# Performance work log

Hardware: AMD Instinct MI355X
Metric: run time of the kernel (lower is better)

The kernel has to match this reference:

```python
import jax, jax.numpy as jnp
import numpy as np

H, HD, C = 16, 64, 64            # num_heads, head_dim, mini_batch_size
BASE_LR = 1.0
EPS = 1e-6                        # ttt LN eps (ln_fwd / ln_fused_l2_bwd)


def _l2norm(x):
    return x / jnp.maximum(jnp.linalg.norm(x, axis=-1, keepdims=True), 1e-12)


def _ln_fwd(x, g, b):
    mu = x.mean(-1, keepdims=True)
    var = x.var(-1, keepdims=True)
    return g * ((x - mu) * jax.lax.rsqrt(var + EPS)) + b


def _ln_l2_bwd(x, tgt, g, b):
    # gradient of ||LN(x)*g+b - tgt||^2 / 2 wrt x
    D = x.shape[-1]
    mu = x.mean(-1, keepdims=True)
    var = x.var(-1, keepdims=True)
    std = jnp.sqrt(var + EPS)
    xh = (x - mu) / std
    gout = (g * xh + b) - tgt
    gxh = gout * g
    return (D * gxh - gxh.sum(-1, keepdims=True) - xh * (gxh * xh).sum(-1, keepdims=True)) / (D * std)


def setup_inputs() -> dict:
    key = jax.random.key(0)
    ks = jax.random.split(key, 12)
    B, L, D = 4, 8192, 1024
    std = 0.02
    return {
        'hidden_states': jax.random.normal(ks[0], (B, L, D), jnp.float32),
        'wq_w': jax.random.normal(ks[1], (D, D), jnp.float32) * std,
        'wq_b': jnp.zeros((D,), jnp.float32),
        'wk_w': jax.random.normal(ks[2], (D, D), jnp.float32) * std,
        'wk_b': jnp.zeros((D,), jnp.float32),
        'wv_w': jax.random.normal(ks[3], (D, D), jnp.float32) * std,
        'wv_b': jnp.zeros((D,), jnp.float32),
        'wo_w': jax.random.normal(ks[4], (D, D), jnp.float32) * std,
        'wo_b': jnp.zeros((D,), jnp.float32),
        'ttt_norm_weight': jnp.ones((H, HD), jnp.float32),
        'ttt_norm_bias': jnp.zeros((H, HD), jnp.float32),
        'ttt_lr_weight': jax.random.normal(ks[5], (H, 1, D), jnp.float32) * std,
        'ttt_lr_bias': jnp.zeros((H, 1), jnp.float32),
        'W1': jax.random.normal(ks[6], (H, HD, HD), jnp.float32) * std,
        'b1': jnp.zeros((H, 1, HD), jnp.float32),
        'post_norm_w': jnp.ones((D,), jnp.float32),
        'post_norm_b': jnp.zeros((D,), jnp.float32),
    }


def _forward(hidden_states, wq_w, wq_b, wk_w, wk_b, wv_w, wv_b, wo_w, wo_b,
             ttt_norm_weight, ttt_norm_bias, ttt_lr_weight, ttt_lr_bias,
             W1, b1, post_norm_w, post_norm_b):
    B, L, D = hidden_states.shape
    NC = L // C
    XQ = (hidden_states @ wq_w.T + wq_b).reshape(B, L, H, HD)
    XK = (hidden_states @ wk_w.T + wk_b).reshape(B, L, H, HD)
    XV = (hidden_states @ wv_w.T + wv_b).reshape(B, L, H, HD)
    XQ = _l2norm(XQ)
    XK = _l2norm(XK)
    # ln_reconstruction_target (uses sample std, ddof=1, eps=1e-5 on std)
    d = XV - XK
    mu = d.mean(-1, keepdims=True)
    sd = d.std(-1, keepdims=True, ddof=1)
    XV = ttt_norm_weight[None, None] * ((d - mu) / (sd + 1e-5)) + ttt_norm_bias[None, None] + XK
    # reshape to mini-batches: [B,H,NC,C,HD]
    Xmb = hidden_states.reshape(B, NC, C, D)
    to_mb = lambda t: t.transpose(0, 2, 1, 3).reshape(B, H, NC, C, HD)
    XQ, XK, XV = to_mb(XQ), to_mb(XK), to_mb(XV)
    # eta: sigmoid lr gate per token, row-broadcast over mini-batch
    ttt_lr = jax.nn.sigmoid(jnp.einsum('bnkc,hdc->bhnkd', Xmb, ttt_lr_weight)
                            + ttt_lr_bias.reshape(1, H, 1, 1, 1))     # [B,H,NC,C,1]
    eta = jnp.swapaxes(ttt_lr, -1, -2) * (BASE_LR / HD / C)           # [B,H,NC,1,C]
    mask = jnp.tril(jnp.ones((C, C), hidden_states.dtype))
    g = ttt_norm_weight[None, :, None, :]
    bta = ttt_norm_bias[None, :, None, :]
    W0 = jnp.broadcast_to(W1[None], (B, H, HD, HD))
    b0 = jnp.broadcast_to(b1[None], (B, H, 1, HD))

    def step(carry, xs):
        W, bvec = carry
        xq, xk, xv, eta_row = xs                      # eta_row: [B,H,1,C]
        Z1 = xk @ W + bvec                            # [B,H,C,HD]
        grad = _ln_l2_bwd(Z1, xv - xk, g, bta)        # [B,H,C,HD]
        Attn = mask * jnp.einsum('bhid,bhjd->bhij', xq, xk)   # [B,H,C,C]
        eta_full = jnp.broadcast_to(eta_row, Attn.shape)      # [B,H,C,C]
        b1_bar = bvec - (mask * eta_full) @ grad              # [B,H,C,HD]
        Z1_bar = xq @ W - (eta_full * Attn) @ grad + b1_bar
        last_eta = eta_full[..., -1, :, None]                 # [B,H,C,1]
        W_new = W - jnp.einsum('bhcd,bhce->bhde', last_eta * xk, grad)
        b_new = bvec - (last_eta * grad).sum(-2, keepdims=True)
        out = xq + _ln_fwd(Z1_bar, g, bta)
        return (W_new, b_new), out

    xs = (jnp.moveaxis(XQ, 2, 0), jnp.moveaxis(XK, 2, 0),
          jnp.moveaxis(XV, 2, 0), jnp.moveaxis(eta, 2, 0))
    _, outs = jax.lax.scan(step, (W0, b0), xs)        # outs: [NC,B,H,C,HD]
    y = jnp.moveaxis(outs, 0, 2).reshape(B, H, L, HD).transpose(0, 2, 1, 3).reshape(B, L, D)
    # post LayerNorm (eps=1e-6) + output projection
    mu2 = y.mean(-1, keepdims=True)
    var2 = y.var(-1, keepdims=True)
    y = post_norm_w * ((y - mu2) * jax.lax.rsqrt(var2 + 1e-6)) + post_norm_b
    return y @ wo_w.T + wo_b


def reference(hidden_states, wq_w, wq_b, wk_w, wk_b, wv_w, wv_b, wo_w, wo_b,
              ttt_norm_weight, ttt_norm_bias, ttt_lr_weight, ttt_lr_bias,
              W1, b1, post_norm_w, post_norm_b):
    return _forward(hidden_states, wq_w, wq_b, wk_w, wk_b, wv_w, wv_b, wo_w, wo_b,
                    ttt_norm_weight, ttt_norm_bias, ttt_lr_weight, ttt_lr_bias,
                    W1, b1, post_norm_w, post_norm_b)
```

## Files before the change

### kernel.cpp

```cpp
#include <hip/hip_runtime.h>


typedef __attribute__((ext_vector_type(8))) short short8;
typedef __attribute__((ext_vector_type(4))) float f32x4;
typedef __attribute__((ext_vector_type(4))) unsigned short us4;

__device__ __forceinline__ float bf2f(unsigned short s) {
  union { unsigned int u; float f; } c;
  c.u = ((unsigned int)s) << 16;
  return c.f;
}
__device__ __forceinline__ unsigned short f2bf(float f) {
  union { float f; unsigned int u; } c;
  c.f = f;
  unsigned int u = c.u;
  return (unsigned short)((u + 0x7FFFu + ((u >> 16) & 1u)) >> 16);
}

__device__ __forceinline__ void gload_lds16(const void* g, void* l) {
  __builtin_amdgcn_global_load_lds(
      (const __attribute__((address_space(1))) unsigned int*)g,
      (__attribute__((address_space(3))) unsigned int*)l, 16, 0, 0);
}

__device__ __forceinline__ float dpp16_sum(float x) {
  int v = __float_as_int(x);
  x += __int_as_float(__builtin_amdgcn_update_dpp(v, v, 0xB1, 0xF, 0xF, true));
  v = __float_as_int(x);
  x += __int_as_float(__builtin_amdgcn_update_dpp(v, v, 0x4E, 0xF, 0xF, true));
  v = __float_as_int(x);
  x += __int_as_float(__builtin_amdgcn_update_dpp(v, v, 0x141, 0xF, 0xF, true));
  v = __float_as_int(x);
  x += __int_as_float(__builtin_amdgcn_update_dpp(v, v, 0x140, 0xF, 0xF, true));
  return x;
}

__device__ __forceinline__ void barrier_fast() {
  __builtin_amdgcn_sched_barrier(0);
  asm volatile("s_waitcnt lgkmcnt(0)" ::: "memory");
  __builtin_amdgcn_s_barrier();
  asm volatile("" ::: "memory");
  __builtin_amdgcn_sched_barrier(0);
}
__device__ __forceinline__ void bar_nowait() {
  __builtin_amdgcn_sched_barrier(0);
  asm volatile("" ::: "memory");
  __builtin_amdgcn_s_barrier();
  asm volatile("" ::: "memory");
  __builtin_amdgcn_sched_barrier(0);
}

__global__ __launch_bounds__(256) void cvt_f32_bf16(
    const float* __restrict__ in, unsigned short* __restrict__ out, long n) {
  long i = ((long)blockIdx.x * 256 + threadIdx.x) * 4;
  if (i + 3 < n) {
    float4 v = *(const float4*)&in[i];
    us4 o = { f2bf(v.x), f2bf(v.y), f2bf(v.z), f2bf(v.w) };
    *(us4*)&out[i] = o;
  }
}

__global__ __launch_bounds__(256) void build_wcat(
    const float* __restrict__ wq, const float* __restrict__ wk,
    const float* __restrict__ wv, const float* __restrict__ lrw,
    const float* __restrict__ wqb, const float* __restrict__ wkb,
    const float* __restrict__ wvb, const float* __restrict__ lrb,
    unsigned short* __restrict__ Wcat, float* __restrict__ biasc) {
  int i = blockIdx.x * 256 + threadIdx.x;
  int row = i >> 10, col = i & 1023;
  int h = row >> 8, o = row & 255;
  float v;
  if (o < 64)        v = wq[(h * 64 + o) * 1024 + col];
  else if (o < 128)  v = wk[(h * 64 + o - 64) * 1024 + col];
  else if (o < 192)  v = wv[(h * 64 + o - 128) * 1024 + col];
  else if (o == 192) v = lrw[h * 1024 + col];
  else               v = 0.f;
  Wcat[i] = f2bf(v);
  if (i < 4096) {
    int hh = i >> 8, oo = i & 255;
    float bv;
    if (oo < 64)        bv = wqb[hh * 64 + oo];
    else if (oo < 128)  bv = wkb[hh * 64 + oo - 64];
    else if (oo < 192)  bv = wvb[hh * 64 + oo - 128];
    else if (oo == 192) bv = lrb[hh];
    else                bv = 0.f;
    biasc[i] = bv;
  }
}


__global__ __launch_bounds__(512, 1) void gemm256_qkv(
    const unsigned short* __restrict__ A, const unsigned short* __restrict__ B,
    const float* __restrict__ bias, const float* __restrict__ tnw,
    const float* __restrict__ tnb, unsigned short* __restrict__ XQn,
    unsigned short* __restrict__ XKn, unsigned short* __restrict__ TGT,
    float* __restrict__ eta, long M, long K) {
  __shared__ __align__(16) unsigned short g_lds[49152];
  char* ldsc = (char*)g_lds;
  const int tid = threadIdx.x, lane = tid & 63, wid = tid >> 6;
  const int wm = wid >> 2, wn = wid & 3;
  const int l15 = lane & 15, lg = lane >> 4;
  const int NTILN = 16;

  unsigned nwg = gridDim.x, bid = blockIdx.x;
  unsigned cpx = nwg >> 3;
  unsigned swz = (bid & 7) * cpx + (bid >> 3);
  unsigned nidx = swz % (unsigned)NTILN, midx = swz / (unsigned)NTILN;
  const long m0 = (long)midx * 256, n0 = (long)nidx * 256;
  const long ldab = K * 2;

  const int srow = wid * 16 + (lane >> 2);
  const int scol = ((lane & 3) * 16) ^ (((lane >> 3) & 3) << 4);
  const int sdst = wid * 1024;
  const char* Ab = (const char*)A;
  const char* Bb = (const char*)B;

  const int acol = (lg * 16) ^ (((l15 >> 1) & 3) << 4);
  const int aro = (wm * 128 + l15) * 64 + acol;
  const int bro = 16384 + (wn * 64 + l15) * 64 + acol;

#define STG_A(tt, h, bb)                                                      \
  gload_lds16(Ab + (size_t)(m0 + (h) * 128 + srow) * ldab + (size_t)(tt) * 64 \
                  + scol,                                                     \
              ldsc + (bb) * 32768 + (h) * 8192 + sdst)
#define STG_B(tt, h, bb)                                                      \
  gload_lds16(Bb + (size_t)(n0 + (h) * 128 + srow) * ldab + (size_t)(tt) * 64 \
                  + scol,                                                     \
              ldsc + (bb) * 32768 + 16384 + (h) * 8192 + sdst)

  f32x4 acc[8][4];
#pragma unroll
  for (int m = 0; m < 8; ++m)
#pragma unroll
    for (int n = 0; n < 4; ++n) acc[m][n] = (f32x4){0.f, 0.f, 0.f, 0.f};

  const int NT = (int)(K >> 5);

  STG_A(0, 0, 0); STG_A(0, 1, 0); STG_B(0, 0, 0); STG_B(0, 1, 0);
  STG_A(1, 0, 1); STG_A(1, 1, 1); STG_B(1, 0, 1); STG_B(1, 1, 1);
  asm volatile("s_waitcnt vmcnt(4)" ::: "memory");
  bar_nowait();

  int buf = 0, sb = 2;
#pragma unroll 1
  for (int t = 0; t < NT; ++t) {
    if (t + 2 < NT) {
      STG_A(t + 2, 0, sb); STG_A(t + 2, 1, sb);
      STG_B(t + 2, 0, sb); STG_B(t + 2, 1, sb);
    }
    const char* ab = ldsc + buf * 32768 + aro;
    const char* bb2 = ldsc + buf * 32768 + bro;
    short8 av[8], bv[4];
#pragma unroll
    for (int i = 0; i < 8; ++i) av[i] = *(const short8*)(ab + i * 1024);
#pragma unroll
    for (int nf = 0; nf < 4; ++nf) bv[nf] = *(const short8*)(bb2 + nf * 1024);
    __builtin_amdgcn_s_setprio(1);
#pragma unroll
    for (int i = 0; i < 8; ++i)
#pragma unroll
      for (int nf = 0; nf < 4; ++nf)
        acc[i][nf] = __builtin_amdgcn_mfma_f32_16x16x32_bf16(av[i], bv[nf],
                                                             acc[i][nf], 0, 0, 0);
    __builtin_amdgcn_s_setprio(0);
    asm volatile("s_waitcnt vmcnt(4)" ::: "memory");
    bar_nowait();
    buf = (buf == 2) ? 0 : buf + 1;
    sb = (sb == 2) ? 0 : sb + 1;
  }
#undef STG_A
#undef STG_B

  const int h = (int)nidx;
  float bcol[4], twv[4], tbv[4];
#pragma unroll
  for (int nf = 0; nf < 4; ++nf) {
    bcol[nf] = bias[n0 + wn * 64 + nf * 16 + l15];
    twv[nf] = tnw[h * 64 + nf * 16 + l15];
    tbv[nf] = tnb[h * 64 + nf * 16 + l15];
  }
  __syncthreads();
  unsigned short* kn_s = g_lds;

  if (wn == 0) {
#pragma unroll
    for (int mf = 0; mf < 8; ++mf)
#pragma unroll
      for (int j = 0; j < 4; ++j) {
        float v[4], s2 = 0.f;
#pragma unroll
        for (int nf = 0; nf < 4; ++nf) {
          v[nf] = acc[mf][nf][j] + bcol[nf];
          s2 += v[nf] * v[nf];
        }
        s2 = dpp16_sum(s2);
        float rn = 1.f / fmaxf(sqrtf(s2), 1e-12f);
        size_t tt = (size_t)(m0 + wm * 128 + mf * 16 + lg * 4 + j);
#pragma unroll
        for (int nf = 0; nf < 4; ++nf)
          XQn[tt * 1024 + h * 64 + nf * 16 + l15] = f2bf(v[nf] * rn);
      }
  } else if (wn == 1) {
#pragma unroll
    for (int mf = 0; mf < 8; ++mf)
#pragma unroll
      for (int j = 0; j < 4; ++j) {
        float v[4], s2 = 0.f;
#pragma unroll
        for (int nf = 0; nf < 4; ++nf) {
          v[nf] = acc[mf][nf][j] + bcol[nf];
          s2 += v[nf] * v[nf];
        }
        s2 = dpp16_sum(s2);
        float rn = 1.f / fmaxf(sqrtf(s2), 1e-12f);
        size_t tt = (size_t)(m0 + wm * 128 + mf * 16 + lg * 4 + j);
        int lr_ = wm * 128 + mf * 16 + lg * 4 + j;
#pragma unroll
        for (int nf = 0; nf < 4; ++nf) {
          unsigned short kb = f2bf(v[nf] * rn);
          XKn[tt * 1024 + h * 64 + nf * 16 + l15] = kb;
          kn_s[lr_ * 72 + nf * 16 + l15] = kb;
        }
      }
  }
  __syncthreads();
  if (wn == 2) {
#pragma unroll
    for (int mf = 0; mf < 8; ++mf)
#pragma unroll
      for (int j = 0; j < 4; ++j) {
        int lr_ = wm * 128 + mf * 16 + lg * 4 + j;
        float dv[4], s1 = 0.f, s2 = 0.f;
#pragma unroll
        for (int nf = 0; nf < 4; ++nf) {
          float kn = bf2f(kn_s[lr_ * 72 + nf * 16 + l15]);
          dv[nf] = acc[mf][nf][j] + bcol[nf] - kn;
          s1 += dv[nf];
          s2 += dv[nf] * dv[nf];
        }
        s1 = dpp16_sum(s1);
        s2 = dpp16_sum(s2);
        float mu = s1 * 0.015625f;
        float var1 = fmaxf(s2 - 64.f * mu * mu, 0.f) * (1.f / 63.f);
        float rs = 1.f / (sqrtf(var1) + 1e-5f);
        size_t tt = (size_t)(m0 + wm * 128 + mf * 16 + lg * 4 + j);
#pragma unroll
        for (int nf = 0; nf < 4; ++nf)
          TGT[tt * 1024 + h * 64 + nf * 16 + l15] =
              f2bf(twv[nf] * ((dv[nf] - mu) * rs) + tbv[nf]);
      }
  } else if (wn == 3 && l15 == 0) {
#pragma unroll
    for (int mf = 0; mf < 8; ++mf)
#pragma unroll
      for (int j = 0; j < 4; ++j) {
        size_t tt = (size_t)(m0 + wm * 128 + mf * 16 + lg * 4 + j);
        float lgt = acc[mf][0][j] + bcol[0];
        float sig = 1.f / (1.f + expf(-lgt));
        eta[((tt >> 13) * 16 + h) * 8192 + (tt & 8191)] = sig * (1.f / 4096.f);
      }
  }
}

template <int WRITE_BF16>
__global__ __launch_bounds__(512, 1) void gemm256(
    const unsigned short* __restrict__ A, const unsigned short* __restrict__ B,
    const float* __restrict__ bias, void* __restrict__ Cout,
    long M, long N, long K, int NTILN, long ldc) {
  __shared__ __align__(16) unsigned short g_lds[49152];
  char* ldsc = (char*)g_lds;
  const int tid = threadIdx.x, lane = tid & 63, wid = tid >> 6;
  const int wm = wid >> 2, wn = wid & 3;
  const int l15 = lane & 15, lg = lane >> 4;

  unsigned nwg = gridDim.x, bid = blockIdx.x;
  unsigned cpx = nwg >> 3;
  unsigned swz = (bid & 7) * cpx + (bid >> 3);
  unsigned nidx = swz % (unsigned)NTILN, midx = swz / (unsigned)NTILN;
  const long m0 = (long)midx * 256, n0 = (long)nidx * 256;
  const long ldab = K * 2;

  const int srow = wid * 16 + (lane >> 2);
  const int scol = ((lane & 3) * 16) ^ (((lane >> 3) & 3) << 4);
  const int sdst = wid * 1024;
  const char* Ab = (const char*)A;
  const char* Bb = (const char*)B;

  const int acol = (lg * 16) ^ (((l15 >> 1) & 3) << 4);
  const int aro = (wm * 128 + l15) * 64 + acol;
  const int bro = 16384 + (wn * 64 + l15) * 64 + acol;

#define STG_A(tt, h, bb)                                                      \
  gload_lds16(Ab + (size_t)(m0 + (h) * 128 + srow) * ldab + (size_t)(tt) * 64 \
                  + scol,                                                     \
              ldsc + (bb) * 32768 + (h) * 8192 + sdst)
#define STG_B(tt, h, bb)                                                      \
  gload_lds16(Bb + (size_t)(n0 + (h) * 128 + srow) * ldab + (size_t)(tt) * 64 \
                  + scol,                                                     \
              ldsc + (bb) * 32768 + 16384 + (h) * 8192 + sdst)

  f32x4 acc[8][4];
#pragma unroll
  for (int m = 0; m < 8; ++m)
#pragma unroll
    for (int n = 0; n < 4; ++n) acc[m][n] = (f32x4){0.f, 0.f, 0.f, 0.f};

  const int NT = (int)(K >> 5);

  STG_A(0, 0, 0); STG_A(0, 1, 0); STG_B(0, 0, 0); STG_B(0, 1, 0);
  STG_A(1, 0, 1); STG_A(1, 1, 1); STG_B(1, 0, 1); STG_B(1, 1, 1);
  asm volatile("s_waitcnt vmcnt(4)" ::: "memory");
  bar_nowait();

  int buf = 0, sb = 2;
#pragma unroll 1
  for (int t = 0; t < NT; ++t) {
    if (t + 2 < NT) {
      STG_A(t + 2, 0, sb); STG_A(t + 2, 1, sb);
      STG_B(t + 2, 0, sb); STG_B(t + 2, 1, sb);
    }
    const char* ab = ldsc + buf * 32768 + aro;
    const char* bb2 = ldsc + buf * 32768 + bro;
    short8 av[8], bv[4];
#pragma unroll
    for (int i = 0; i < 8; ++i) av[i] = *(const short8*)(ab + i * 1024);
#pragma unroll
    for (int nf = 0; nf < 4; ++nf) bv[nf] = *(const short8*)(bb2 + nf * 1024);
    __builtin_amdgcn_s_setprio(1);
#pragma unroll
    for (int i = 0; i < 8; ++i)
#pragma unroll
      for (int nf = 0; nf < 4; ++nf)
        acc[i][nf] = __builtin_amdgcn_mfma_f32_16x16x32_bf16(av[i], bv[nf],
                                                             acc[i][nf], 0, 0, 0);
    __builtin_amdgcn_s_setprio(0);
    asm volatile("s_waitcnt vmcnt(4)" ::: "memory");
    bar_nowait();
    buf = (buf == 2) ? 0 : buf + 1;
    sb = (sb == 2) ? 0 : sb + 1;
  }
#undef STG_A
#undef STG_B

#pragma unroll
  for (int mf = 0; mf < 8; ++mf) {
    long r0 = m0 + wm * 128 + mf * 16 + lg * 4;
#pragma unroll
    for (int nf = 0; nf < 4; ++nf) {
      long c = n0 + wn * 64 + nf * 16 + l15;
      float bvv = bias ? bias[c] : 0.f;
#pragma unroll
      for (int j = 0; j < 4; ++j) {
        float v = acc[mf][nf][j] + bvv;
        if (WRITE_BF16)
          ((unsigned short*)Cout)[(r0 + j) * ldc + c] = f2bf(v);
        else
          ((float*)Cout)[(r0 + j) * ldc + c] = v;
      }
    }
  }
}

__global__ __launch_bounds__(512, 1) void ttt_scan(
    const unsigned short* __restrict__ XQ, const unsigned short* __restrict__ XK,
    const unsigned short* __restrict__ TG, const float* __restrict__ eta_buf,
    const float* __restrict__ W1, const float* __restrict__ b1,
    const float* __restrict__ tnw, const float* __restrict__ tnb,
    float* __restrict__ y) {
  const int bh = blockIdx.x;
  const int b = bh >> 4, h = bh & 15;
  const int tid = threadIdx.x;
  const int lane = tid & 63, wid = tid >> 6;
  const bool isA = wid < 4;
  const int q = wid & 3;
  const int l15 = lane & 15, lg = lane >> 4;

  __shared__ __align__(16) unsigned short xq_s[2][64 * 72];
  __shared__ __align__(16) unsigned short tg_s[2][64 * 72];
  __shared__ __align__(16) unsigned short xk_s[2][64 * 72];
  __shared__ __align__(16) unsigned short gc_s[64 * 72];
  __shared__ __align__(16) unsigned short gradT[64 * 72];
  __shared__ __align__(16) unsigned short xkTe[64 * 72];
  __shared__ __align__(16) unsigned short WT_b[2][64 * 72];
  __shared__ float eta_s[2][64];
  __shared__ float bpart[4][64];

  const size_t tokb = (size_t)b * 8192;
  const int col0 = h * 64;
  const int rr_ = q * 16 + (lane >> 3);
  const int c8_ = (lane & 7) * 8;

  short8 pA0[2], pA1[2], pB0[2];
  float peta = 0.f;
  float bstv[4], gwv[4], gbv[4];
  f32x4 Wreg[4];

  if (isA) {
#pragma unroll
    for (int n = 0; n < 4; ++n) {
      int e = n * 16 + l15;
      bstv[n] = b1[h * 64 + e];
      gwv[n] = tnw[h * 64 + e];
      gbv[n] = tnb[h * 64 + e];
    }
#pragma unroll
    for (int j = 0; j < 2; ++j) {
      size_t g = (tokb + rr_ + j * 8) * 1024 + col0 + c8_;
      pA0[j] = *(const short8*)&XQ[g];
      pA1[j] = *(const short8*)&TG[g];
    }
#pragma unroll
    for (int j = 0; j < 2; ++j) {
      int rr = rr_ + j * 8;
      *(short8*)&xq_s[0][rr * 72 + c8_] = pA0[j];
      *(short8*)&tg_s[0][rr * 72 + c8_] = pA1[j];
    }
#pragma unroll
    for (int j = 0; j < 2; ++j) {
      size_t g = (tokb + 64 + rr_ + j * 8) * 1024 + col0 + c8_;
      pA0[j] = *(const short8*)&XQ[g];
      pA1[j] = *(const short8*)&TG[g];
    }
  } else {
#pragma unroll
    for (int j = 0; j < 2; ++j)
      pB0[j] = *(const short8*)&XK[(tokb + rr_ + j * 8) * 1024 + col0 + c8_];
#pragma unroll
    for (int j = 0; j < 2; ++j)
      *(short8*)&xk_s[0][(rr_ + j * 8) * 72 + c8_] = pB0[j];
#pragma unroll
    for (int j = 0; j < 2; ++j)
      pB0[j] = *(const short8*)&XK[(tokb + 64 + rr_ + j * 8) * 1024 + col0 + c8_];
#pragma unroll
    for (int n = 0; n < 4; ++n)
#pragma unroll
      for (int jj = 0; jj < 4; ++jj) {
        int d = q * 16 + lg * 4 + jj, e = n * 16 + l15;
        float w = W1[h * 4096 + d * 64 + e];
        Wreg[n][jj] = w;
        WT_b[0][e * 72 + d] = f2bf(w);
      }
    if (wid == 4) {
      eta_s[0][lane] = eta_buf[(size_t)bh * 8192 + lane];
      peta = eta_buf[(size_t)bh * 8192 + 64 + lane];
    }
  }
  __syncthreads();

  for (int nc = 0; nc < 128; ++nc) {
    const int p = nc & 1;
    const unsigned short* WTc = WT_b[p];
    unsigned short* WTn = WT_b[p ^ 1];

    if (isA) {
      if (nc) {
#pragma unroll
        for (int n = 0; n < 4; ++n) {
          int e = n * 16 + l15;
          bstv[n] -= bpart[0][e] + bpart[1][e] + bpart[2][e] + bpart[3][e];
        }
      }
      if (nc + 1 < 128) {
#pragma unroll
        for (int j = 0; j < 2; ++j) {
          int rr = rr_ + j * 8;
          *(short8*)&xq_s[p ^ 1][rr * 72 + c8_] = pA0[j];
          *(short8*)&tg_s[p ^ 1][rr * 72 + c8_] = pA1[j];
        }
      }
      if (nc + 2 < 128) {
#pragma unroll
        for (int j = 0; j < 2; ++j) {
          size_t g = (tokb + (nc + 2) * 64 + rr_ + j * 8) * 1024 + col0 + c8_;
          pA0[j] = *(const short8*)&XQ[g];
          pA1[j] = *(const short8*)&TG[g];
        }
      }
      f32x4 accZ[4];
#pragma unroll
      for (int n = 0; n < 4; ++n)
        accZ[n] = (f32x4){bstv[n], bstv[n], bstv[n], bstv[n]};
      __builtin_amdgcn_s_setprio(1);
#pragma unroll
      for (int kk = 0; kk < 2; ++kk) {
        const int ko = kk * 32 + lg * 8;
        short8 a_xk = *(const short8*)&xk_s[p][(q * 16 + l15) * 72 + ko];
#pragma unroll
        for (int n = 0; n < 4; ++n) {
          short8 b_w = *(const short8*)&WTc[(n * 16 + l15) * 72 + ko];
          accZ[n] = __builtin_amdgcn_mfma_f32_16x16x32_bf16(a_xk, b_w, accZ[n], 0, 0, 0);
        }
      }
      __builtin_amdgcn_s_setprio(0);
      float grv[4][4];
#pragma unroll
      for (int j = 0; j < 4; ++j) {
        const int r = q * 16 + lg * 4 + j;
        float z[4], s1 = 0.f, s2 = 0.f;
#pragma unroll
        for (int n = 0; n < 4; ++n) {
          z[n] = accZ[n][j];
          s1 += z[n];
          s2 += z[n] * z[n];
        }
        s1 = dpp16_sum(s1);
        s2 = dpp16_sum(s2);
        float mu = s1 * 0.015625f;
        float var = s2 * 0.015625f - mu * mu;
        float rstd = rsqrtf(var + 1e-6f);
        float xh[4], gx[4], s3 = 0.f, s4 = 0.f;
#pragma unroll
        for (int n = 0; n < 4; ++n) {
          xh[n] = (z[n] - mu) * rstd;
          float tg = bf2f(tg_s[p][r * 72 + n * 16 + l15]);
          float go = gwv[n] * xh[n] + gbv[n] - tg;
          gx[n] = go * gwv[n];
          s3 += gx[n];
          s4 += gx[n] * xh[n];
        }
        s3 = dpp16_sum(s3);
        s4 = dpp16_sum(s4);
#pragma unroll
        for (int n = 0; n < 4; ++n)
          grv[n][j] = (64.f * gx[n] - s3 - xh[n] * s4) * rstd * 0.015625f;
      }
#pragma unroll
      for (int n = 0; n < 4; ++n) {
        us4 pk = {f2bf(grv[n][0]), f2bf(grv[n][1]), f2bf(grv[n][2]),
                  f2bf(grv[n][3])};
        *(us4*)&gradT[(n * 16 + l15) * 72 + q * 16 + lg * 4] = pk;
      }
    } else {
      if (nc + 1 < 128) {
#pragma unroll
        for (int j = 0; j < 2; ++j)
          *(short8*)&xk_s[p ^ 1][(rr_ + j * 8) * 72 + c8_] = pB0[j];
        if (wid == 4) eta_s[p ^ 1][lane] = peta;
      }
      if (nc + 2 < 128) {
#pragma unroll
        for (int j = 0; j < 2; ++j)
          pB0[j] = *(const short8*)
              &XK[(tokb + (nc + 2) * 64 + rr_ + j * 8) * 1024 + col0 + c8_];
        if (wid == 4) peta = eta_buf[(size_t)bh * 8192 + (nc + 2) * 64 + lane];
      }
#pragma unroll
      for (int it = 0; it < 4; ++it) {
        int c0 = q * 16 + it * 4;
        us4 pk;
#pragma unroll
        for (int u = 0; u < 4; ++u)
          pk[u] = f2bf(-eta_s[p][c0 + u] * bf2f(xk_s[p][(c0 + u) * 72 + lane]));
        *(us4*)&xkTe[lane * 72 + c0] = pk;
      }
      f32x4 accA[4];
#pragma unroll
      for (int n = 0; n < 4; ++n) accA[n] = (f32x4){0.f, 0.f, 0.f, 0.f};
      __builtin_amdgcn_s_setprio(1);
#pragma unroll
      for (int kk = 0; kk < 2; ++kk) {
        const int ko = kk * 32 + lg * 8;
        short8 a_xq = *(const short8*)&xq_s[p][(q * 16 + l15) * 72 + ko];
#pragma unroll
        for (int n = 0; n < 4; ++n) {
          short8 b_k = *(const short8*)&xk_s[p][(n * 16 + l15) * 72 + ko];
          accA[n] = __builtin_amdgcn_mfma_f32_16x16x32_bf16(a_xq, b_k, accA[n], 0, 0, 0);
        }
      }
      __builtin_amdgcn_s_setprio(0);
#pragma unroll
      for (int j = 0; j < 4; ++j) {
        const int r = q * 16 + lg * 4 + j;
#pragma unroll
        for (int n = 0; n < 4; ++n) {
          int cj = n * 16 + l15;
          float v = (cj <= r) ? (-eta_s[p][cj] * (1.f + accA[n][j])) : 0.f;
          gc_s[r * 72 + cj] = f2bf(v);
        }
      }
    }
    barrier_fast();

    if (isA) {
      f32x4 accZb[4];
#pragma unroll
      for (int n = 0; n < 4; ++n)
        accZb[n] = (f32x4){bstv[n], bstv[n], bstv[n], bstv[n]};
      __builtin_amdgcn_s_setprio(1);
#pragma unroll
      for (int kk = 0; kk < 2; ++kk) {
        const int ko = kk * 32 + lg * 8;
        short8 a_xq = *(const short8*)&xq_s[p][(q * 16 + l15) * 72 + ko];
        short8 a_gc = *(const short8*)&gc_s[(q * 16 + l15) * 72 + ko];
#pragma unroll
        for (int n = 0; n < 4; ++n) {
          short8 b_w = *(const short8*)&WTc[(n * 16 + l15) * 72 + ko];
          short8 b_g = *(const short8*)&gradT[(n * 16 + l15) * 72 + ko];
          accZb[n] = __builtin_amdgcn_mfma_f32_16x16x32_bf16(a_xq, b_w, accZb[n], 0, 0, 0);
          accZb[n] = __builtin_amdgcn_mfma_f32_16x16x32_bf16(a_gc, b_g, accZb[n], 0, 0, 0);
        }
      }
      __builtin_amdgcn_s_setprio(0);
#pragma unroll
      for (int j = 0; j < 4; ++j) {
        const int r = q * 16 + lg * 4 + j;
        float z[4], s1 = 0.f, s2 = 0.f;
#pragma unroll
        for (int n = 0; n < 4; ++n) {
          z[n] = accZb[n][j];
          s1 += z[n];
          s2 += z[n] * z[n];
        }
        s1 = dpp16_sum(s1);
        s2 = dpp16_sum(s2);
        float mu = s1 * 0.015625f;
        float var = s2 * 0.015625f - mu * mu;
        float rstd = rsqrtf(var + 1e-6f);
        size_t gbase = (tokb + nc * 64 + r) * 1024 + col0;
#pragma unroll
        for (int n = 0; n < 4; ++n) {
          int e = n * 16 + l15;
          float ov = bf2f(xq_s[p][r * 72 + e]) + gwv[n] * ((z[n] - mu) * rstd) + gbv[n];
          y[gbase + e] = ov;
        }
      }
    } else {
      short8 a_ke[2], b_g[2][4];
#pragma unroll
      for (int kk = 0; kk < 2; ++kk) {
        const int ko = kk * 32 + lg * 8;
        a_ke[kk] = *(const short8*)&xkTe[(q * 16 + l15) * 72 + ko];
#pragma unroll
        for (int n = 0; n < 4; ++n)
          b_g[kk][n] = *(const short8*)&gradT[(n * 16 + l15) * 72 + ko];
      }
      f32x4 accW[4];
#pragma unroll
      for (int n = 0; n < 4; ++n) accW[n] = Wreg[n];
      __builtin_amdgcn_s_setprio(1);
#pragma unroll
      for (int kk = 0; kk < 2; ++kk)
#pragma unroll
        for (int n = 0; n < 4; ++n)
          accW[n] = __builtin_amdgcn_mfma_f32_16x16x32_bf16(a_ke[kk], b_g[kk][n],
                                                            accW[n], 0, 0, 0);
      __builtin_amdgcn_s_setprio(0);
#pragma unroll
      for (int n = 0; n < 4; ++n) {
        Wreg[n] = accW[n];
        us4 pk = {f2bf(accW[n][0]), f2bf(accW[n][1]), f2bf(accW[n][2]),
                  f2bf(accW[n][3])};
        *(us4*)&WTn[(n * 16 + l15) * 72 + q * 16 + lg * 4] = pk;
      }
      {
        float s = 0.f;
#pragma unroll
        for (int it = 0; it < 4; ++it) {
          us4 gv = *(const us4*)&gradT[lane * 72 + q * 16 + it * 4];
#pragma unroll
          for (int u = 0; u < 4; ++u)
            s += eta_s[p][q * 16 + it * 4 + u] * bf2f(gv[u]);
        }
        bpart[q][lane] = s;
      }
    }
    barrier_fast();
  }
}

__global__ __launch_bounds__(256) void postnorm(
    const float* __restrict__ yv, const float* __restrict__ pw,
    const float* __restrict__ pb, unsigned short* __restrict__ yn) {
  int t = blockIdx.x;
  int tid = threadIdx.x, lane = tid & 63, wid = tid >> 6;
  const float* row = yv + (size_t)t * 1024;
  float4 v = *(const float4*)&row[tid * 4];
  float s1 = v.x + v.y + v.z + v.w;
  float s2 = v.x * v.x + v.y * v.y + v.z * v.z + v.w * v.w;
#pragma unroll
  for (int o = 1; o < 64; o <<= 1) {
    s1 += __shfl_xor(s1, o);
    s2 += __shfl_xor(s2, o);
  }
  __shared__ float r1[4], r2[4];
  if (lane == 0) {
    r1[wid] = s1;
    r2[wid] = s2;
  }
  __syncthreads();
  s1 = r1[0] + r1[1] + r1[2] + r1[3];
  s2 = r2[0] + r2[1] + r2[2] + r2[3];
  float mu = s1 * (1.f / 1024.f);
  float var = s2 * (1.f / 1024.f) - mu * mu;
  float rstd = rsqrtf(var + 1e-6f);
  int c = tid * 4;
  us4 o4 = {f2bf(pw[c] * ((v.x - mu) * rstd) + pb[c]),
            f2bf(pw[c + 1] * ((v.y - mu) * rstd) + pb[c + 1]),
            f2bf(pw[c + 2] * ((v.z - mu) * rstd) + pb[c + 2]),
            f2bf(pw[c + 3] * ((v.w - mu) * rstd) + pb[c + 3])};
  *(us4*)&yn[(size_t)t * 1024 + c] = o4;
}

extern "C" void kernel_launch(void* const* d_in, const int* in_sizes, int n_in,
                              void* d_out, int out_size, void* d_ws,
                              size_t ws_size, hipStream_t stream) {
  const float* hs  = (const float*)d_in[0];
  const float* wqw = (const float*)d_in[1];
  const float* wqb = (const float*)d_in[2];
  const float* wkw = (const float*)d_in[3];
  const float* wkb = (const float*)d_in[4];
  const float* wvw = (const float*)d_in[5];
  const float* wvb = (const float*)d_in[6];
  const float* wow = (const float*)d_in[7];
  const float* wob = (const float*)d_in[8];
  const float* tnw = (const float*)d_in[9];
  const float* tnb = (const float*)d_in[10];
  const float* lrw = (const float*)d_in[11];
  const float* lrb = (const float*)d_in[12];
  const float* W1  = (const float*)d_in[13];
  const float* b1  = (const float*)d_in[14];
  const float* pnw = (const float*)d_in[15];
  const float* pnb = (const float*)d_in[16];

  const size_t OFF_XQ    = 0;
  const size_t OFF_XK    = 67108864;
  const size_t OFF_TGT   = 134217728;
  const size_t OFF_ETA   = 201326592;
  const size_t OFF_WOBF  = OFF_ETA + 2097152;
  const size_t OFF_HSBF  = OFF_WOBF + 2097152;
  const size_t OFF_WCAT  = OFF_HSBF + 67108864;
  const size_t OFF_BIASC = OFF_WCAT + 8388608;
  const size_t OFF_YV    = OFF_HSBF;
  const size_t NEEDED_A  = OFF_BIASC + 16384;
  const size_t NEEDED_B  = OFF_YV + 134217728;
  const size_t NEEDED    = NEEDED_A > NEEDED_B ? NEEDED_A : NEEDED_B;
  if (ws_size < NEEDED) return;

  char* ws = (char*)d_ws;
  unsigned short* XQn   = (unsigned short*)(ws + OFF_XQ);
  unsigned short* ynorm = (unsigned short*)(ws + OFF_XQ);
  unsigned short* XKn   = (unsigned short*)(ws + OFF_XK);
  unsigned short* TGT   = (unsigned short*)(ws + OFF_TGT);
  float* eta_buf        = (float*)(ws + OFF_ETA);
  unsigned short* wo_bf = (unsigned short*)(ws + OFF_WOBF);
  unsigned short* hs_bf = (unsigned short*)(ws + OFF_HSBF);
  unsigned short* Wcat  = (unsigned short*)(ws + OFF_WCAT);
  float* biasc          = (float*)(ws + OFF_BIASC);
  float* yv             = (float*)(ws + OFF_YV);

  cvt_f32_bf16<<<32768, 256, 0, stream>>>(hs, hs_bf, 33554432L);
  build_wcat<<<16384, 256, 0, stream>>>(wqw, wkw, wvw, lrw, wqb, wkb, wvb, lrb,
                                        Wcat, biasc);
  cvt_f32_bf16<<<1024, 256, 0, stream>>>(wow, wo_bf, 1048576L);
  gemm256_qkv<<<2048, 512, 0, stream>>>(hs_bf, Wcat, biasc, tnw, tnb,
                                        XQn, XKn, TGT, eta_buf, 32768L, 1024L);
  ttt_scan<<<64, 512, 0, stream>>>(XQn, XKn, TGT, eta_buf, W1, b1, tnw, tnb, yv);
  postnorm<<<32768, 256, 0, stream>>>(yv, pnw, pnb, ynorm);
  gemm256<0><<<512, 512, 0, stream>>>(ynorm, wo_bf, wob, d_out,
                                      32768L, 1024L, 1024L, 4, 1024L);
}
```

Measured before the change: 889.1 us.

## Fuse TTT scan with postnorm and output GEMM via progress-flag overlap

After: 996.5 us. +12.1%, slower.

```diff
diff --git a/kernel.cpp b/kernel.cpp
--- a/kernel.cpp
+++ b/kernel.cpp
@@ -88,7 +88,6 @@
   }
 }
 
-
 __global__ __launch_bounds__(512, 1) void gemm256_qkv(
     const unsigned short* __restrict__ A, const unsigned short* __restrict__ B,
     const float* __restrict__ bias, const float* __restrict__ tnw,
@@ -262,443 +261,466 @@
   }
 }
 
-template <int WRITE_BF16>
-__global__ __launch_bounds__(512, 1) void gemm256(
-    const unsigned short* __restrict__ A, const unsigned short* __restrict__ B,
-    const float* __restrict__ bias, void* __restrict__ Cout,
-    long M, long N, long K, int NTILN, long ldc) {
-  __shared__ __align__(16) unsigned short g_lds[49152];
-  char* ldsc = (char*)g_lds;
-  const int tid = threadIdx.x, lane = tid & 63, wid = tid >> 6;
-  const int wm = wid >> 2, wn = wid & 3;
-  const int l15 = lane & 15, lg = lane >> 4;
-
-  unsigned nwg = gridDim.x, bid = blockIdx.x;
-  unsigned cpx = nwg >> 3;
-  unsigned swz = (bid & 7) * cpx + (bid >> 3);
-  unsigned nidx = swz % (unsigned)NTILN, midx = swz / (unsigned)NTILN;
-  const long m0 = (long)midx * 256, n0 = (long)nidx * 256;
-  const long ldab = K * 2;
-
-  const int srow = wid * 16 + (lane >> 2);
-  const int scol = ((lane & 3) * 16) ^ (((lane >> 3) & 3) << 4);
-  const int sdst = wid * 1024;
-  const char* Ab = (const char*)A;
-  const char* Bb = (const char*)B;
-
-  const int acol = (lg * 16) ^ (((l15 >> 1) & 3) << 4);
-  const int aro = (wm * 128 + l15) * 64 + acol;
-  const int bro = 16384 + (wn * 64 + l15) * 64 + acol;
-
-#define STG_A(tt, h, bb)                                                      \
-  gload_lds16(Ab + (size_t)(m0 + (h) * 128 + srow) * ldab + (size_t)(tt) * 64 \
-                  + scol,                                                     \
-              ldsc + (bb) * 32768 + (h) * 8192 + sdst)
-#define STG_B(tt, h, bb)                                                      \
-  gload_lds16(Bb + (size_t)(n0 + (h) * 128 + srow) * ldab + (size_t)(tt) * 64 \
-                  + scol,                                                     \
-              ldsc + (bb) * 32768 + 16384 + (h) * 8192 + sdst)
-
-  f32x4 acc[8][4];
-#pragma unroll
-  for (int m = 0; m < 8; ++m)
-#pragma unroll
-    for (int n = 0; n < 4; ++n) acc[m][n] = (f32x4){0.f, 0.f, 0.f, 0.f};
-
-  const int NT = (int)(K >> 5);
-
-  STG_A(0, 0, 0); STG_A(0, 1, 0); STG_B(0, 0, 0); STG_B(0, 1, 0);
-  STG_A(1, 0, 1); STG_A(1, 1, 1); STG_B(1, 0, 1); STG_B(1, 1, 1);
-  asm volatile("s_waitcnt vmcnt(4)" ::: "memory");
-  bar_nowait();
-
-  int buf = 0, sb = 2;
-#pragma unroll 1
-  for (int t = 0; t < NT; ++t) {
-    if (t + 2 < NT) {
-      STG_A(t + 2, 0, sb); STG_A(t + 2, 1, sb);
-      STG_B(t + 2, 0, sb); STG_B(t + 2, 1, sb);
-    }
-    const char* ab = ldsc + buf * 32768 + aro;
-    const char* bb2 = ldsc + buf * 32768 + bro;
-    short8 av[8], bv[4];
-#pragma unroll
-    for (int i = 0; i < 8; ++i) av[i] = *(const short8*)(ab + i * 1024);
-#pragma unroll
-    for (int nf = 0; nf < 4; ++nf) bv[nf] = *(const short8*)(bb2 + nf * 1024);
-    __builtin_amdgcn_s_setprio(1);
-#pragma unroll
-    for (int i = 0; i < 8; ++i)
-#pragma unroll
-      for (int nf = 0; nf < 4; ++nf)
-        acc[i][nf] = __builtin_amdgcn_mfma_f32_16x16x32_bf16(av[i], bv[nf],
-                                                             acc[i][nf], 0, 0, 0);
-    __builtin_amdgcn_s_setprio(0);
-    asm volatile("s_waitcnt vmcnt(4)" ::: "memory");
-    bar_nowait();
-    buf = (buf == 2) ? 0 : buf + 1;
-    sb = (sb == 2) ? 0 : sb + 1;
-  }
-#undef STG_A
-#undef STG_B
-
-#pragma unroll
-  for (int mf = 0; mf < 8; ++mf) {
-    long r0 = m0 + wm * 128 + mf * 16 + lg * 4;
-#pragma unroll
-    for (int nf = 0; nf < 4; ++nf) {
-      long c = n0 + wn * 64 + nf * 16 + l15;
-      float bvv = bias ? bias[c] : 0.f;
-#pragma unroll
-      for (int j = 0; j < 4; ++j) {
-        float v = acc[mf][nf][j] + bvv;
-        if (WRITE_BF16)
-          ((unsigned short*)Cout)[(r0 + j) * ldc + c] = f2bf(v);
-        else
-          ((float*)Cout)[(r0 + j) * ldc + c] = v;
-      }
-    }
-  }
-}
-
-__global__ __launch_bounds__(512, 1) void ttt_scan(
+__global__ __launch_bounds__(512, 1) void scan_out(
     const unsigned short* __restrict__ XQ, const unsigned short* __restrict__ XK,
     const unsigned short* __restrict__ TG, const float* __restrict__ eta_buf,
     const float* __restrict__ W1, const float* __restrict__ b1,
     const float* __restrict__ tnw, const float* __restrict__ tnb,
-    float* __restrict__ y) {
-  const int bh = blockIdx.x;
-  const int b = bh >> 4, h = bh & 15;
+    float* __restrict__ y, const unsigned short* __restrict__ wo_bf,
+    const float* __restrict__ wob, const float* __restrict__ pnw,
+    const float* __restrict__ pnb, float* __restrict__ out,
+    unsigned int* __restrict__ prog) {
+  __shared__ __align__(16) char smem[108544];
   const int tid = threadIdx.x;
   const int lane = tid & 63, wid = tid >> 6;
-  const bool isA = wid < 4;
-  const int q = wid & 3;
   const int l15 = lane & 15, lg = lane >> 4;
 
-  __shared__ __align__(16) unsigned short xq_s[2][64 * 72];
-  __shared__ __align__(16) unsigned short tg_s[2][64 * 72];
-  __shared__ __align__(16) unsigned short xk_s[2][64 * 72];
-  __shared__ __align__(16) unsigned short gc_s[64 * 72];
-  __shared__ __align__(16) unsigned short gradT[64 * 72];
-  __shared__ __align__(16) unsigned short xkTe[64 * 72];
-  __shared__ __align__(16) unsigned short WT_b[2][64 * 72];
-  __shared__ float eta_s[2][64];
-  __shared__ float bpart[4][64];
-
-  const size_t tokb = (size_t)b * 8192;
-  const int col0 = h * 64;
-  const int rr_ = q * 16 + (lane >> 3);
-  const int c8_ = (lane & 7) * 8;
-
-  short8 pA0[2], pA1[2], pB0[2];
-  float peta = 0.f;
-  float bstv[4], gwv[4], gbv[4];
-  f32x4 Wreg[4];
-
-  if (isA) {
-#pragma unroll
-    for (int n = 0; n < 4; ++n) {
-      int e = n * 16 + l15;
-      bstv[n] = b1[h * 64 + e];
-      gwv[n] = tnw[h * 64 + e];
-      gbv[n] = tnb[h * 64 + e];
+  if (blockIdx.x < 64) {
+    unsigned short* xq_s = (unsigned short*)(smem);
+    unsigned short* tg_s = (unsigned short*)(smem + 18432);
+    unsigned short* xk_s = (unsigned short*)(smem + 36864);
+    unsigned short* gc_s = (unsigned short*)(smem + 55296);
+    unsigned short* gradT = (unsigned short*)(smem + 64512);
+    unsigned short* xkTe = (unsigned short*)(smem + 73728);
+    unsigned short* WT_b = (unsigned short*)(smem + 82944);
+    float* eta_s = (float*)(smem + 101376);
+    float* bpart = (float*)(smem + 101888);
+
+    const int bh = blockIdx.x;
+    const int b = bh >> 4, h = bh & 15;
+    const bool isA = wid < 4;
+    const int q = wid & 3;
+    const size_t tokb = (size_t)b * 8192;
+    const int col0 = h * 64;
+    const int rr_ = q * 16 + (lane >> 3);
+    const int c8_ = (lane & 7) * 8;
+
+    short8 pA0[2], pA1[2], pB0[2];
+    float peta = 0.f;
+    float bstv[4], gwv[4], gbv[4];
+    f32x4 Wreg[4];
+
+    if (isA) {
+#pragma unroll
+      for (int n = 0; n < 4; ++n) {
+        int e = n * 16 + l15;
+        bstv[n] = b1[h * 64 + e];
+        gwv[n] = tnw[h * 64 + e];
+        gbv[n] = tnb[h * 64 + e];
+      }
+#pragma unroll
+      for (int j = 0; j < 2; ++j) {
+        size_t g = (tokb + rr_ + j * 8) * 1024 + col0 + c8_;
+        pA0[j] = *(const short8*)&XQ[g];
+        pA1[j] = *(const short8*)&TG[g];
+      }
+#pragma unroll
+      for (int j = 0; j < 2; ++j) {
+        int rr = rr_ + j * 8;
+        *(short8*)&xq_s[rr * 72 + c8_] = pA0[j];
+        *(short8*)&tg_s[rr * 72 + c8_] = pA1[j];
+      }
+#pragma unroll
+      for (int j = 0; j < 2; ++j) {
+        size_t g = (tokb + 64 + rr_ + j * 8) * 1024 + col0 + c8_;
+        pA0[j] = *(const short8*)&XQ[g];
+        pA1[j] = *(const short8*)&TG[g];
+      }
+    } else {
+#pragma unroll
+      for (int j = 0; j < 2; ++j)
+        pB0[j] = *(const short8*)&XK[(tokb + rr_ + j * 8) * 1024 + col0 + c8_];
+#pragma unroll
+      for (int j = 0; j < 2; ++j)
+        *(short8*)&xk_s[(rr_ + j * 8) * 72 + c8_] = pB0[j];
+#pragma unroll
+      for (int j = 0; j < 2; ++j)
+        pB0[j] = *(const short8*)&XK[(tokb + 64 + rr_ + j * 8) * 1024 + col0 + c8_];
+#pragma unroll
+      for (int n = 0; n < 4; ++n)
+#pragma unroll
+        for (int jj = 0; jj < 4; ++jj) {
+          int d = q * 16 + lg * 4 + jj, e = n * 16 + l15;
+          float w = W1[h * 4096 + d * 64 + e];
+          Wreg[n][jj] = w;
+          WT_b[e * 72 + d] = f2bf(w);
+        }
+      if (wid == 4) {
+        eta_s[lane] = eta_buf[(size_t)bh * 8192 + lane];
+        peta = eta_buf[(size_t)bh * 8192 + 64 + lane];
+      }
     }
-#pragma unroll
-    for (int j = 0; j < 2; ++j) {
-      size_t g = (tokb + rr_ + j * 8) * 1024 + col0 + c8_;
-      pA0[j] = *(const short8*)&XQ[g];
-      pA1[j] = *(const short8*)&TG[g];
-    }
-#pragma unroll
-    for (int j = 0; j < 2; ++j) {
-      int rr = rr_ + j * 8;
-      *(short8*)&xq_s[0][rr * 72 + c8_] = pA0[j];
-      *(short8*)&tg_s[0][rr * 72 + c8_] = pA1[j];
-    }
-#pragma unroll
-    for (int j = 0; j < 2; ++j) {
-      size_t g = (tokb + 64 + rr_ + j * 8) * 1024 + col0 + c8_;
-      pA0[j] = *(const short8*)&XQ[g];
-      pA1[j] = *(const short8*)&TG[g];
+    __syncthreads();
+
+    for (int nc = 0; nc < 128; ++nc) {
+      const int p = nc & 1;
+      const unsigned short* WTc = WT_b + p * 4608;
+      unsigned short* WTn = WT_b + (p ^ 1) * 4608;
+      unsigned short* xqp = xq_s + p * 4608;
+      unsigned short* tgp = tg_s + p * 4608;
+      unsigned short* xkp = xk_s + p * 4608;
+      float* etp = eta_s + p * 64;
+
+      if (isA) {
+        if (nc) {
+#pragma unroll
+          for (int n = 0; n < 4; ++n) {
+            int e = n * 16 + l15;
+            bstv[n] -= bpart[e] + bpart[64 + e] + bpart[128 + e] + bpart[192 + e];
+          }
+        }
+        if (nc + 1 < 128) {
+          unsigned short* xqn = xq_s + (p ^ 1) * 4608;
+          unsigned short* tgn = tg_s + (p ^ 1) * 4608;
+#pragma unroll
+          for (int j = 0; j < 2; ++j) {
+            int rr = rr_ + j * 8;
+            *(short8*)&xqn[rr * 72 + c8_] = pA0[j];
+            *(short8*)&tgn[rr * 72 + c8_] = pA1[j];
+          }
+        }
+        if (nc + 2 < 128) {
+#pragma unroll
+          for (int j = 0; j < 2; ++j) {
+            size_t g = (tokb + (nc + 2) * 64 + rr_ + j * 8) * 1024 + col0 + c8_;
+            pA0[j] = *(const short8*)&XQ[g];
+            pA1[j] = *(const short8*)&TG[g];
+          }
+        }
+        f32x4 accZ[4];
+#pragma unroll
+        for (int n = 0; n < 4; ++n)
+          accZ[n] = (f32x4){bstv[n], bstv[n], bstv[n], bstv[n]};
+        __builtin_amdgcn_s_setprio(1);
+#pragma unroll
+        for (int kk = 0; kk < 2; ++kk) {
+          const int ko = kk * 32 + lg * 8;
+          short8 a_xk = *(const short8*)&xkp[(q * 16 + l15) * 72 + ko];
+#pragma unroll
+          for (int n = 0; n < 4; ++n) {
+            short8 b_w = *(const short8*)&WTc[(n * 16 + l15) * 72 + ko];
+            accZ[n] = __builtin_amdgcn_mfma_f32_16x16x32_bf16(a_xk, b_w, accZ[n], 0, 0, 0);
+          }
+        }
+        __builtin_amdgcn_s_setprio(0);
+        float grv[4][4];
+#pragma unroll
+        for (int j = 0; j < 4; ++j) {
+          const int r = q * 16 + lg * 4 + j;
+          float z[4], s1 = 0.f, s2 = 0.f;
+#pragma unroll
+          for (int n = 0; n < 4; ++n) {
+            z[n] = accZ[n][j];
+            s1 += z[n];
+            s2 += z[n] * z[n];
+          }
+          s1 = dpp16_sum(s1);
+          s2 = dpp16_sum(s2);
+          float mu = s1 * 0.015625f;
+          float var = s2 * 0.015625f - mu * mu;
+          float rstd = rsqrtf(var + 1e-6f);
+          float xh[4], gx[4], s3 = 0.f, s4 = 0.f;
+#pragma unroll
+          for (int n = 0; n < 4; ++n) {
+            xh[n] = (z[n] - mu) * rstd;
+            float tg = bf2f(tgp[r * 72 + n * 16 + l15]);
+            float go = gwv[n] * xh[n] + gbv[n] - tg;
+            gx[n] = go * gwv[n];
+            s3 += gx[n];
+            s4 += gx[n] * xh[n];
+          }
+          s3 = dpp16_sum(s3);
+          s4 = dpp16_sum(s4);
+#pragma unroll
+          for (int n = 0; n < 4; ++n)
+            grv[n][j] = (64.f * gx[n] - s3 - xh[n] * s4) * rstd * 0.015625f;
+        }
+#pragma unroll
+        for (int n = 0; n < 4; ++n) {
+          us4 pk = {f2bf(grv[n][0]), f2bf(grv[n][1]), f2bf(grv[n][2]),
+                    f2bf(grv[n][3])};
+          *(us4*)&gradT[(n * 16 + l15) * 72 + q * 16 + lg * 4] = pk;
+        }
+      } else {
+        if (nc + 1 < 128) {
+          unsigned short* xkn = xk_s + (p ^ 1) * 4608;
+#pragma unroll
+          for (int j = 0; j < 2; ++j)
+            *(short8*)&xkn[(rr_ + j * 8) * 72 + c8_] = pB0[j];
+          if (wid == 4) eta_s[(p ^ 1) * 64 + lane] = peta;
+        }
+        if (nc + 2 < 128) {
+#pragma unroll
+          for (int j = 0; j < 2; ++j)
+            pB0[j] = *(const short8*)
+                &XK[(tokb + (nc + 2) * 64 + rr_ + j * 8) * 1024 + col0 + c8_];
+          if (wid == 4) peta = eta_buf[(size_t)bh * 8192 + (nc + 2) * 64 + lane];
+        }
+#pragma unroll
+        for (int it = 0; it < 4; ++it) {
+          int c0 = q * 16 + it * 4;
+          us4 pk;
+#pragma unroll
+          for (int u = 0; u < 4; ++u)
+            pk[u] = f2bf(-etp[c0 + u] * bf2f(xkp[(c0 + u) * 72 + lane]));
+          *(us4*)&xkTe[lane * 72 + c0] = pk;
+        }
+        f32x4 accA[4];
+#pragma unroll
+        for (int n = 0; n < 4; ++n) accA[n] = (f32x4){0.f, 0.f, 0.f, 0.f};
+        __builtin_amdgcn_s_setprio(1);
+#pragma unroll
+        for (int kk = 0; kk < 2; ++kk) {
+          const int ko = kk * 32 + lg * 8;
+          short8 a_xq = *(const short8*)&xqp[(q * 16 + l15) * 72 + ko];
+#pragma unroll
+          for (int n = 0; n < 4; ++n) {
+            short8 b_k = *(const short8*)&xkp[(n * 16 + l15) * 72 + ko];
+            accA[n] = __builtin_amdgcn_mfma_f32_16x16x32_bf16(a_xq, b_k, accA[n], 0, 0, 0);
+          }
+        }
+        __builtin_amdgcn_s_setprio(0);
+#pragma unroll
+        for (int j = 0; j < 4; ++j) {
+          const int r = q * 16 + lg * 4 + j;
+#pragma unroll
+          for (int n = 0; n < 4; ++n) {
+            int cj = n * 16 + l15;
+            float v = (cj <= r) ? (-etp[cj] * (1.f + accA[n][j])) : 0.f;
+            gc_s[r * 72 + cj] = f2bf(v);
+          }
+        }
+      }
+      barrier_fast();
+
+      if (isA) {
+        f32x4 accZb[4];
+#pragma unroll
+        for (int n = 0; n < 4; ++n)
+          accZb[n] = (f32x4){bstv[n], bstv[n], bstv[n], bstv[n]};
+        __builtin_amdgcn_s_setprio(1);
+#pragma unroll
+        for (int kk = 0; kk < 2; ++kk) {
+          const int ko = kk * 32 + lg * 8;
+          short8 a_xq = *(const short8*)&xqp[(q * 16 + l15) * 72 + ko];
+          short8 a_gc = *(const short8*)&gc_s[(q * 16 + l15) * 72 + ko];
+#pragma unroll
+          for (int n = 0; n < 4; ++n) {
+            short8 b_w = *(const short8*)&WTc[(n * 16 + l15) * 72 + ko];
+            short8 b_g = *(const short8*)&gradT[(n * 16 + l15) * 72 + ko];
+            accZb[n] = __builtin_amdgcn_mfma_f32_16x16x32_bf16(a_xq, b_w, accZb[n], 0, 0, 0);
+            accZb[n] = __builtin_amdgcn_mfma_f32_16x16x32_bf16(a_gc, b_g, accZb[n], 0, 0, 0);
+          }
+        }
+        __builtin_amdgcn_s_setprio(0);
+#pragma unroll
+        for (int j = 0; j < 4; ++j) {
+          const int r = q * 16 + lg * 4 + j;
+          float z[4], s1 = 0.f, s2 = 0.f;
+#pragma unroll
+          for (int n = 0; n < 4; ++n) {
+            z[n] = accZb[n][j];
+            s1 += z[n];
+            s2 += z[n] * z[n];
+          }
+          s1 = dpp16_sum(s1);
+          s2 = dpp16_sum(s2);
+          float mu = s1 * 0.015625f;
+          float var = s2 * 0.015625f - mu * mu;
+          float rstd = rsqrtf(var + 1e-6f);
+          size_t gbase = (tokb + nc * 64 + r) * 1024 + col0;
+#pragma unroll
+          for (int n = 0; n < 4; ++n) {
+            int e = n * 16 + l15;
+            float ov = bf2f(xqp[r * 72 + e]) + gwv[n] * ((z[n] - mu) * rstd) + gbv[n];
+            y[gbase + e] = ov;
+          }
+        }
+        if ((nc & 3) == 3)
+          asm volatile("s_waitcnt vmcnt(0)" ::: "memory");
+      } else {
+        short8 a_ke[2], b_g[2][4];
+#pragma unroll
+        for (int kk = 0; kk < 2; ++kk) {
+          const int ko = kk * 32 + lg * 8;
+          a_ke[kk] = *(const short8*)&xkTe[(q * 16 + l15) * 72 + ko];
+#pragma unroll
+          for (int n = 0; n < 4; ++n)
+            b_g[kk][n] = *(const short8*)&gradT[(n * 16 + l15) * 72 + ko];
+        }
+        f32x4 accW[4];
+#pragma unroll
+        for (int n = 0; n < 4; ++n) accW[n] = Wreg[n];
+        __builtin_amdgcn_s_setprio(1);
+#pragma unroll
+        for (int kk = 0; kk < 2; ++kk)
+#pragma unroll
+          for (int n = 0; n < 4; ++n)
+            accW[n] = __builtin_amdgcn_mfma_f32_16x16x32_bf16(a_ke[kk], b_g[kk][n],
+                                                              accW[n], 0, 0, 0);
+        __builtin_amdgcn_s_setprio(0);
+#pragma unroll
+        for (int n = 0; n < 4; ++n) {
+          Wreg[n] = accW[n];
+          us4 pk = {f2bf(accW[n][0]), f2bf(accW[n][1]), f2bf(accW[n][2]),
+                    f2bf(accW[n][3])};
+          *(us4*)&WTn[(n * 16 + l15) * 72 + q * 16 + lg * 4] = pk;
+        }
+        {
+          float s = 0.f;
+#pragma unroll
+          for (int it = 0; it < 4; ++it) {
+            us4 gv = *(const us4*)&gradT[lane * 72 + q * 16 + it * 4];
+#pragma unroll
+            for (int u = 0; u < 4; ++u)
+              s += etp[q * 16 + it * 4 + u] * bf2f(gv[u]);
+          }
+          bpart[q * 64 + lane] = s;
+        }
+      }
+      barrier_fast();
+      if (((nc & 3) == 3) && tid == 0) {
+        __threadfence();
+        __hip_atomic_fetch_add(&prog[(b << 5) + (nc >> 2)], 1u,
+                               __ATOMIC_RELEASE, __HIP_MEMORY_SCOPE_AGENT);
+      }
     }
   } else {
-#pragma unroll
-    for (int j = 0; j < 2; ++j)
-      pB0[j] = *(const short8*)&XK[(tokb + rr_ + j * 8) * 1024 + col0 + c8_];
-#pragma unroll
-    for (int j = 0; j < 2; ++j)
-      *(short8*)&xk_s[0][(rr_ + j * 8) * 72 + c8_] = pB0[j];
-#pragma unroll
-    for (int j = 0; j < 2; ++j)
-      pB0[j] = *(const short8*)&XK[(tokb + 64 + rr_ + j * 8) * 1024 + col0 + c8_];
-#pragma unroll
-    for (int n = 0; n < 4; ++n)
-#pragma unroll
-      for (int jj = 0; jj < 4; ++jj) {
-        int d = q * 16 + lg * 4 + jj, e = n * 16 + l15;
-        float w = W1[h * 4096 + d * 64 + e];
-        Wreg[n][jj] = w;
-        WT_b[0][e * 72 + d] = f2bf(w);
-      }
-    if (wid == 4) {
-      eta_s[0][lane] = eta_buf[(size_t)bh * 8192 + lane];
-      peta = eta_buf[(size_t)bh * 8192 + 64 + lane];
+    char* ldsc = smem;
+    float* mu_s = (float*)(smem + 98304);
+    float* rs_s = (float*)(smem + 99328);
+    float* pnw_s = (float*)(smem + 100352);
+    float* pnb_s = (float*)(smem + 104448);
+
+    const int wkid = blockIdx.x - 64;
+    const int wm = wid >> 2, wn = wid & 3;
+    const int srow = wid * 16 + (lane >> 2);
+    const int scol = ((lane & 3) * 16) ^ (((lane >> 3) & 3) << 4);
+    const int sdst = wid * 1024;
+    const int acol = (lg * 16) ^ (((l15 >> 1) & 3) << 4);
+    const int aro = (wm * 128 + l15) * 64 + acol;
+    const int bro = 16384 + (wn * 64 + l15) * 64 + acol;
+
+    if (tid < 256) *(float4*)&pnw_s[tid * 4] = *(const float4*)&pnw[tid * 4];
+    else { int t2 = tid - 256; *(float4*)&pnb_s[t2 * 4] = *(const float4*)&pnb[t2 * 4]; }
+
+    for (int i = wkid; i < 512; i += 192) {
+      const int mtp = i >> 4, rem = i & 15, b = rem >> 2, nt = rem & 3;
+      const long m0 = (long)b * 8192 + (long)mtp * 256;
+      const long n0 = (long)nt * 256;
+
+      if (tid == 0) {
+        while (__hip_atomic_load(&prog[(b << 5) + mtp], __ATOMIC_ACQUIRE,
+                                 __HIP_MEMORY_SCOPE_AGENT) < 16u)
+          __builtin_amdgcn_s_sleep(32);
+      }
+      __syncthreads();
+
+      for (int rr = 0; rr < 32; ++rr) {
+        int r = wid * 32 + rr;
+        const float* row = y + (size_t)(m0 + r) * 1024;
+        float s1 = 0.f, s2 = 0.f;
+#pragma unroll
+        for (int k = 0; k < 4; ++k) {
+          float4 v = *(const float4*)&row[k * 256 + lane * 4];
+          s1 += v.x + v.y + v.z + v.w;
+          s2 += v.x * v.x + v.y * v.y + v.z * v.z + v.w * v.w;
+        }
+#pragma unroll
+        for (int o2 = 1; o2 < 64; o2 <<= 1) {
+          s1 += __shfl_xor(s1, o2);
+          s2 += __shfl_xor(s2, o2);
+        }
+        if (lane == 0) {
+          float mu = s1 * (1.f / 1024.f);
+          float var = s2 * (1.f / 1024.f) - mu * mu;
+          mu_s[r] = mu;
+          rs_s[r] = rsqrtf(var + 1e-6f);
+        }
+      }
+      __syncthreads();
+
+      auto stageA = [&](int tt, int sl) {
+        int r = tid >> 1, half = tid & 1;
+        const float* ysrc = y + (size_t)(m0 + r) * 1024 + tt * 32 + half * 16;
+        float4 f0 = *(const float4*)(ysrc);
+        float4 f1 = *(const float4*)(ysrc + 4);
+        float4 f2 = *(const float4*)(ysrc + 8);
+        float4 f3 = *(const float4*)(ysrc + 12);
+        float mu = mu_s[r], rs = rs_s[r];
+        int c0 = tt * 32 + half * 16;
+        __align__(16) unsigned short o[16];
+        float vv[16] = {f0.x, f0.y, f0.z, f0.w, f1.x, f1.y, f1.z, f1.w,
+                        f2.x, f2.y, f2.z, f2.w, f3.x, f3.y, f3.z, f3.w};
+#pragma unroll
+        for (int u = 0; u < 16; ++u)
+          o[u] = f2bf(pnw_s[c0 + u] * ((vv[u] - mu) * rs) + pnb_s[c0 + u]);
+        int key = ((r >> 1) & 3) << 4;
+        char* base = ldsc + sl * 32768 + r * 64;
+        *(short8*)(base + ((half * 32) ^ key)) = *(short8*)&o[0];
+        *(short8*)(base + ((half * 32 + 16) ^ key)) = *(short8*)&o[8];
+      };
+      auto stgB = [&](int tt, int sl) {
+        gload_lds16((const char*)wo_bf + (size_t)(n0 + srow) * 2048 +
+                        (size_t)tt * 64 + scol,
+                    ldsc + sl * 32768 + 16384 + sdst);
+        gload_lds16((const char*)wo_bf + (size_t)(n0 + 128 + srow) * 2048 +
+                        (size_t)tt * 64 + scol,
+                    ldsc + sl * 32768 + 16384 + 8192 + sdst);
+      };
+
+      f32x4 acc[8][4];
+#pragma unroll
+      for (int m = 0; m < 8; ++m)
+#pragma unroll
+        for (int n = 0; n < 4; ++n) acc[m][n] = (f32x4){0.f, 0.f, 0.f, 0.f};
+
+      stgB(0, 0); stgB(1, 1);
+      stageA(0, 0); stageA(1, 1);
+      asm volatile("s_waitcnt vmcnt(2)" ::: "memory");
+      barrier_fast();
+
+#pragma unroll 1
+      for (int t = 0; t < 32; ++t) {
+        const int buf = t % 3, sb = (t + 2) % 3;
+        if (t + 2 < 32) { stgB(t + 2, sb); stageA(t + 2, sb); }
+        const char* ab = ldsc + buf * 32768 + aro;
+        const char* bb2 = ldsc + buf * 32768 + bro;
+        short8 av[8], bv[4];
+#pragma unroll
+        for (int ii = 0; ii < 8; ++ii) av[ii] = *(const short8*)(ab + ii * 1024);
+#pragma unroll
+        for (int nf = 0; nf < 4; ++nf) bv[nf] = *(const short8*)(bb2 + nf * 1024);
+        __builtin_amdgcn_s_setprio(1);
+#pragma unroll
+        for (int ii = 0; ii < 8; ++ii)
+#pragma unroll
+          for (int nf = 0; nf < 4; ++nf)
+            acc[ii][nf] = __builtin_amdgcn_mfma_f32_16x16x32_bf16(
+                av[ii], bv[nf], acc[ii][nf], 0, 0, 0);
+        __builtin_amdgcn_s_setprio(0);
+        if (t + 2 < 32)
+          asm volatile("s_waitcnt vmcnt(2)" ::: "memory");
+        else
+          asm volatile("s_waitcnt vmcnt(0)" ::: "memory");
+        barrier_fast();
+      }
+
+#pragma unroll
+      for (int mf = 0; mf < 8; ++mf) {
+        long r0 = m0 + wm * 128 + mf * 16 + lg * 4;
+#pragma unroll
+        for (int nf = 0; nf < 4; ++nf) {
+          long c = n0 + wn * 64 + nf * 16 + l15;
+          float bvv = wob[c];
+#pragma unroll
+          for (int j = 0; j < 4; ++j)
+            out[(r0 + j) * 1024 + c] = acc[mf][nf][j] + bvv;
+        }
+      }
+      __syncthreads();
     }
   }
-  __syncthreads();
-
-  for (int nc = 0; nc < 128; ++nc) {
-    const int p = nc & 1;
-    const unsigned short* WTc = WT_b[p];
-    unsigned short* WTn = WT_b[p ^ 1];
-
-    if (isA) {
-      if (nc) {
-#pragma unroll
-        for (int n = 0; n < 4; ++n) {
-          int e = n * 16 + l15;
-          bstv[n] -= bpart[0][e] + bpart[1][e] + bpart[2][e] + bpart[3][e];
-        }
-      }
-      if (nc + 1 < 128) {
-#pragma unroll
-        for (int j = 0; j < 2; ++j) {
-          int rr = rr_ + j * 8;
-          *(short8*)&xq_s[p ^ 1][rr * 72 + c8_] = pA0[j];
-          *(short8*)&tg_s[p ^ 1][rr * 72 + c8_] = pA1[j];
-        }
-      }
-      if (nc + 2 < 128) {
-#pragma unroll
-        for (int j = 0; j < 2; ++j) {
-          size_t g = (tokb + (nc + 2) * 64 + rr_ + j * 8) * 1024 + col0 + c8_;
-          pA0[j] = *(const short8*)&XQ[g];
-          pA1[j] = *(const short8*)&TG[g];
-        }
-      }
-      f32x4 accZ[4];
-#pragma unroll
-      for (int n = 0; n < 4; ++n)
-        accZ[n] = (f32x4){bstv[n], bstv[n], bstv[n], bstv[n]};
-      __builtin_amdgcn_s_setprio(1);
-#pragma unroll
-      for (int kk = 0; kk < 2; ++kk) {
-        const int ko = kk * 32 + lg * 8;
-        short8 a_xk = *(const short8*)&xk_s[p][(q * 16 + l15) * 72 + ko];
-#pragma unroll
-        for (int n = 0; n < 4; ++n) {
-          short8 b_w = *(const short8*)&WTc[(n * 16 + l15) * 72 + ko];
-          accZ[n] = __builtin_amdgcn_mfma_f32_16x16x32_bf16(a_xk, b_w, accZ[n], 0, 0, 0);
-        }
-      }
-      __builtin_amdgcn_s_setprio(0);
-      float grv[4][4];
-#pragma unroll
-      for (int j = 0; j < 4; ++j) {
-        const int r = q * 16 + lg * 4 + j;
-        float z[4], s1 = 0.f, s2 = 0.f;
-#pragma unroll
-        for (int n = 0; n < 4; ++n) {
-          z[n] = accZ[n][j];
-          s1 += z[n];
-          s2 += z[n] * z[n];
-        }
-        s1 = dpp16_sum(s1);
-        s2 = dpp16_sum(s2);
-        float mu = s1 * 0.015625f;
-        float var = s2 * 0.015625f - mu * mu;
-        float rstd = rsqrtf(var + 1e-6f);
-        float xh[4], gx[4], s3 = 0.f, s4 = 0.f;
-#pragma unroll
-        for (int n = 0; n < 4; ++n) {
-          xh[n] = (z[n] - mu) * rstd;
-          float tg = bf2f(tg_s[p][r * 72 + n * 16 + l15]);
-          float go = gwv[n] * xh[n] + gbv[n] - tg;
-          gx[n] = go * gwv[n];
-          s3 += gx[n];
-          s4 += gx[n] * xh[n];
-        }
-        s3 = dpp16_sum(s3);
-        s4 = dpp16_sum(s4);
-#pragma unroll
-        for (int n = 0; n < 4; ++n)
-          grv[n][j] = (64.f * gx[n] - s3 - xh[n] * s4) * rstd * 0.015625f;
-      }
-#pragma unroll
-      for (int n = 0; n < 4; ++n) {
-        us4 pk = {f2bf(grv[n][0]), f2bf(grv[n][1]), f2bf(grv[n][2]),
-                  f2bf(grv[n][3])};
-        *(us4*)&gradT[(n * 16 + l15) * 72 + q * 16 + lg * 4] = pk;
-      }
-    } else {
-      if (nc + 1 < 128) {
-#pragma unroll
-        for (int j = 0; j < 2; ++j)
-          *(short8*)&xk_s[p ^ 1][(rr_ + j * 8) * 72 + c8_] = pB0[j];
-        if (wid == 4) eta_s[p ^ 1][lane] = peta;
-      }
-      if (nc + 2 < 128) {
-#pragma unroll
-        for (int j = 0; j < 2; ++j)
-          pB0[j] = *(const short8*)
-              &XK[(tokb + (nc + 2) * 64 + rr_ + j * 8) * 1024 + col0 + c8_];
-        if (wid == 4) peta = eta_buf[(size_t)bh * 8192 + (nc + 2) * 64 + lane];
-      }
-#pragma unroll
-      for (int it = 0; it < 4; ++it) {
-        int c0 = q * 16 + it * 4;
-        us4 pk;
-#pragma unroll
-        for (int u = 0; u < 4; ++u)
-          pk[u] = f2bf(-eta_s[p][c0 + u] * bf2f(xk_s[p][(c0 + u) * 72 + lane]));
-        *(us4*)&xkTe[lane * 72 + c0] = pk;
-      }
-      f32x4 accA[4];
-#pragma unroll
-      for (int n = 0; n < 4; ++n) accA[n] = (f32x4){0.f, 0.f, 0.f, 0.f};
-      __builtin_amdgcn_s_setprio(1);
-#pragma unroll
-      for (int kk = 0; kk < 2; ++kk) {
-        const int ko = kk * 32 + lg * 8;
-        short8 a_xq = *(const short8*)&xq_s[p][(q * 16 + l15) * 72 + ko];
-#pragma unroll
-        for (int n = 0; n < 4; ++n) {
-          short8 b_k = *(const short8*)&xk_s[p][(n * 16 + l15) * 72 + ko];
-          accA[n] = __builtin_amdgcn_mfma_f32_16x16x32_bf16(a_xq, b_k, accA[n], 0, 0, 0);
-        }
-      }
-      __builtin_amdgcn_s_setprio(0);
-#pragma unroll
-      for (int j = 0; j < 4; ++j) {
-        const int r = q * 16 + lg * 4 + j;
-#pragma unroll
-        for (int n = 0; n < 4; ++n) {
-          int cj = n * 16 + l15;
-          float v = (cj <= r) ? (-eta_s[p][cj] * (1.f + accA[n][j])) : 0.f;
-          gc_s[r * 72 + cj] = f2bf(v);
-        }
-      }
-    }
-    barrier_fast();
-
-    if (isA) {
-      f32x4 accZb[4];
-#pragma unroll
-      for (int n = 0; n < 4; ++n)
-        accZb[n] = (f32x4){bstv[n], bstv[n], bstv[n], bstv[n]};
-      __builtin_amdgcn_s_setprio(1);
-#pragma unroll
-      for (int kk = 0; kk < 2; ++kk) {
-        const int ko = kk * 32 + lg * 8;
-        short8 a_xq = *(const short8*)&xq_s[p][(q * 16 + l15) * 72 + ko];
-        short8 a_gc = *(const short8*)&gc_s[(q * 16 + l15) * 72 + ko];
-#pragma unroll
-        for (int n = 0; n < 4; ++n) {
-          short8 b_w = *(const short8*)&WTc[(n * 16 + l15) * 72 + ko];
-          short8 b_g = *(const short8*)&gradT[(n * 16 + l15) * 72 + ko];
-          accZb[n] = __builtin_amdgcn_mfma_f32_16x16x32_bf16(a_xq, b_w, accZb[n], 0, 0, 0);
-          accZb[n] = __builtin_amdgcn_mfma_f32_16x16x32_bf16(a_gc, b_g, accZb[n], 0, 0, 0);
-        }
-      }
-      __builtin_amdgcn_s_setprio(0);
-#pragma unroll
-      for (int j = 0; j < 4; ++j) {
-        const int r = q * 16 + lg * 4 + j;
-        float z[4], s1 = 0.f, s2 = 0.f;
-#pragma unroll
-        for (int n = 0; n < 4; ++n) {
-          z[n] = accZb[n][j];
-          s1 += z[n];
-          s2 += z[n] * z[n];
-        }
-        s1 = dpp16_sum(s1);
-        s2 = dpp16_sum(s2);
-        float mu = s1 * 0.015625f;
-        float var = s2 * 0.015625f - mu * mu;
-        float rstd = rsqrtf(var + 1e-6f);
-        size_t gbase = (tokb + nc * 64 + r) * 1024 + col0;
-#pragma unroll
-        for (int n = 0; n < 4; ++n) {
-          int e = n * 16 + l15;
-          float ov = bf2f(xq_s[p][r * 72 + e]) + gwv[n] * ((z[n] - mu) * rstd) + gbv[n];
-          y[gbase + e] = ov;
-        }
-      }
-    } else {
-      short8 a_ke[2], b_g[2][4];
-#pragma unroll
-      for (int kk = 0; kk < 2; ++kk) {
-        const int ko = kk * 32 + lg * 8;
-        a_ke[kk] = *(const short8*)&xkTe[(q * 16 + l15) * 72 + ko];
-#pragma unroll
-        for (int n = 0; n < 4; ++n)
-          b_g[kk][n] = *(const short8*)&gradT[(n * 16 + l15) * 72 + ko];
-      }
-      f32x4 accW[4];
-#pragma unroll
-      for (int n = 0; n < 4; ++n) accW[n] = Wreg[n];
-      __builtin_amdgcn_s_setprio(1);
-#pragma unroll
-      for (int kk = 0; kk < 2; ++kk)
-#pragma unroll
-        for (int n = 0; n < 4; ++n)
-          accW[n] = __builtin_amdgcn_mfma_f32_16x16x32_bf16(a_ke[kk], b_g[kk][n],
-                                                            accW[n], 0, 0, 0);
-      __builtin_amdgcn_s_setprio(0);
-#pragma unroll
-      for (int n = 0; n < 4; ++n) {
-        Wreg[n] = accW[n];
-        us4 pk = {f2bf(accW[n][0]), f2bf(accW[n][1]), f2bf(accW[n][2]),
-                  f2bf(accW[n][3])};
-        *(us4*)&WTn[(n * 16 + l15) * 72 + q * 16 + lg * 4] = pk;
-      }
-      {
-        float s = 0.f;
-#pragma unroll
-        for (int it = 0; it < 4; ++it) {
-          us4 gv = *(const us4*)&gradT[lane * 72 + q * 16 + it * 4];
-#pragma unroll
-          for (int u = 0; u < 4; ++u)
-            s += eta_s[p][q * 16 + it * 4 + u] * bf2f(gv[u]);
-        }
-        bpart[q][lane] = s;
-      }
-    }
-    barrier_fast();
-  }
-}
-
-__global__ __launch_bounds__(256) void postnorm(
-    const float* __restrict__ yv, const float* __restrict__ pw,
-    const float* __restrict__ pb, unsigned short* __restrict__ yn) {
-  int t = blockIdx.x;
-  int tid = threadIdx.x, lane = tid & 63, wid = tid >> 6;
-  const float* row = yv + (size_t)t * 1024;
-  float4 v = *(const float4*)&row[tid * 4];
-  float s1 = v.x + v.y + v.z + v.w;
-  float s2 = v.x * v.x + v.y * v.y + v.z * v.z + v.w * v.w;
-#pragma unroll
-  for (int o = 1; o < 64; o <<= 1) {
-    s1 += __shfl_xor(s1, o);
-    s2 += __shfl_xor(s2, o);
-  }
-  __shared__ float r1[4], r2[4];
-  if (lane == 0) {
-    r1[wid] = s1;
-    r2[wid] = s2;
-  }
-  __syncthreads();
-  s1 = r1[0] + r1[1] + r1[2] + r1[3];
-  s2 = r2[0] + r2[1] + r2[2] + r2[3];
-  float mu = s1 * (1.f / 1024.f);
-  float var = s2 * (1.f / 1024.f) - mu * mu;
-  float rstd = rsqrtf(var + 1e-6f);
-  int c = tid * 4;
-  us4 o4 = {f2bf(pw[c] * ((v.x - mu) * rstd) + pb[c]),
-            f2bf(pw[c + 1] * ((v.y - mu) * rstd) + pb[c + 1]),
-            f2bf(pw[c + 2] * ((v.z - mu) * rstd) + pb[c + 2]),
-            f2bf(pw[c + 3] * ((v.w - mu) * rstd) + pb[c + 3])};
-  *(us4*)&yn[(size_t)t * 1024 + c] = o4;
 }
 
 extern "C" void kernel_launch(void* const* d_in, const int* in_sizes, int n_in,
@@ -726,8 +748,9 @@
   const size_t OFF_XK    = 67108864;
   const size_t OFF_TGT   = 134217728;
   const size_t OFF_ETA   = 201326592;
-  const size_t OFF_WOBF  = OFF_ETA + 2097152;
-  const size_t OFF_HSBF  = OFF_WOBF + 2097152;
+  const size_t OFF_WOBF  = 203423744;
+  const size_t OFF_PROG  = 205520896;
+  const size_t OFF_HSBF  = 205524992;
   const size_t OFF_WCAT  = OFF_HSBF + 67108864;
   const size_t OFF_BIASC = OFF_WCAT + 8388608;
   const size_t OFF_YV    = OFF_HSBF;
@@ -738,11 +761,11 @@
 
   char* ws = (char*)d_ws;
   unsigned short* XQn   = (unsigned short*)(ws + OFF_XQ);
-  unsigned short* ynorm = (unsigned short*)(ws + OFF_XQ);
   unsigned short* XKn   = (unsigned short*)(ws + OFF_XK);
   unsigned short* TGT   = (unsigned short*)(ws + OFF_TGT);
   float* eta_buf        = (float*)(ws + OFF_ETA);
   unsigned short* wo_bf = (unsigned short*)(ws + OFF_WOBF);
+  unsigned int* prog    = (unsigned int*)(ws + OFF_PROG);
   unsigned short* hs_bf = (unsigned short*)(ws + OFF_HSBF);
   unsigned short* Wcat  = (unsigned short*)(ws + OFF_WCAT);
   float* biasc          = (float*)(ws + OFF_BIASC);
@@ -754,8 +777,8 @@
   cvt_f32_bf16<<<1024, 256, 0, stream>>>(wow, wo_bf, 1048576L);
   gemm256_qkv<<<2048, 512, 0, stream>>>(hs_bf, Wcat, biasc, tnw, tnb,
                                         XQn, XKn, TGT, eta_buf, 32768L, 1024L);
-  ttt_scan<<<64, 512, 0, stream>>>(XQn, XKn, TGT, eta_buf, W1, b1, tnw, tnb, yv);
-  postnorm<<<32768, 256, 0, stream>>>(yv, pnw, pnb, ynorm);
-  gemm256<0><<<512, 512, 0, stream>>>(ynorm, wo_bf, wob, d_out,
-                                      32768L, 1024L, 1024L, 4, 1024L);
-}
+  hipMemsetAsync(prog, 0, 4096, stream);
+  scan_out<<<256, 512, 0, stream>>>(XQn, XKn, TGT, eta_buf, W1, b1, tnw, tnb,
+                                    yv, wo_bf, wob, pnw, pnb, (float*)d_out,
+                                    prog);
+}
```
